# Kernel tuning notes

Hardware: AMD Instinct MI355X
Metric: run time of the kernel (lower is better)

The kernel has to match this reference:

```python
import jax, jax.numpy as jnp
import numpy as np

THETA = 10000.0

def _rope_cos_sin(seq_len, head_dim, dtype=jnp.float32):
    # matches precompute_freqs_cis: freqs over even indices of head_dim
    inv = 1.0 / (THETA ** (jnp.arange(0, head_dim, 2, dtype=jnp.float32) / head_dim))  # [hd/2]
    ang = jnp.arange(seq_len, dtype=jnp.float32)[:, None] * inv[None, :]               # [S, hd/2]
    return jnp.cos(ang).astype(dtype), jnp.sin(ang).astype(dtype)

def _apply_rope(x, cos, sin):
    # x: [b, h, s, d]; pairs are interleaved (d r) with r=2 -> complex (even=real, odd=imag)
    xe = x[..., 0::2]
    xo = x[..., 1::2]
    re = xe * cos - xo * sin
    im = xe * sin + xo * cos
    # interleave back: [..., d/2, 2] -> [..., d]
    return jnp.stack([re, im], axis=-1).reshape(x.shape)

def setup_inputs() -> dict:
    key = jax.random.key(0)
    ks = jax.random.split(key, 8)
    B, S, D = 2, 2048, 1024
    s = 0.02
    return {
        "query": jax.random.normal(ks[0], (B, S, D), jnp.float32),
        "key": jax.random.normal(ks[1], (B, S, D), jnp.float32),
        "value": jax.random.normal(ks[2], (B, S, D), jnp.float32),
        "q_w": jax.random.normal(ks[3], (D, D), jnp.float32) * s,
        "q_b": jnp.zeros((D,), jnp.float32),
        "k_w": jax.random.normal(ks[4], (D, D), jnp.float32) * s,
        "k_b": jnp.zeros((D,), jnp.float32),
        "v_w": jax.random.normal(ks[5], (D, D), jnp.float32) * s,
        "v_b": jnp.zeros((D,), jnp.float32),
        "o_w": jax.random.normal(ks[6], (D, D), jnp.float32) * s,
        "o_b": jnp.zeros((D,), jnp.float32),
    }

def reference(query, key, value, q_w, q_b, k_w, k_b, v_w, v_b, o_w, o_b):
    H = 16
    B, S, D = query.shape
    hd = D // H
    scaling = hd ** -0.5

    def split_heads(x):  # [b, s, (h d)] -> [b, h, s, d]
        return x.reshape(B, -1, H, hd).transpose(0, 2, 1, 3)

    q = split_heads(query @ q_w.T + q_b)
    k = split_heads(key @ k_w.T + k_b)
    v = split_heads(value @ v_w.T + v_b)

    cos, sin = _rope_cos_sin(S, hd)
    q = _apply_rope(q, cos, sin)
    k = _apply_rope(k, cos, sin)

    scores = jnp.einsum('bhqd,bhkd->bhqk', q, k) * scaling  # [B,H,S,S]
    attn = jax.nn.softmax(scores, axis=-1)
    out = jnp.einsum('bhqk,bhkd->bhqd', attn, v)            # [B,H,S,hd]
    out = out.transpose(0, 2, 1, 3).reshape(B, S, D)
    return out @ o_w.T + o_b
```

## Files before the change

### kernel.cpp

```cpp
#include <hip/hip_runtime.h>
#include <math.h>

#define B_  2
#define S_  2048
#define D_  1024
#define H_  16
#define HD_ 64
#define M_  (B_*S_)

typedef __attribute__((ext_vector_type(8))) short bf16x8;
typedef __attribute__((ext_vector_type(4))) short bf16x4;
typedef __attribute__((ext_vector_type(4))) float f32x4;
typedef unsigned short ushort_t;

#define MFMA32 __builtin_amdgcn_mfma_f32_16x16x32_bf16
#define MFMA16 __builtin_amdgcn_mfma_f32_16x16x16bf16_1k

__device__ inline unsigned short f2bf(float x) {
    unsigned u = __float_as_uint(x);
    unsigned r = (u + 0x7fff + ((u >> 16) & 1)) >> 16;
    return (unsigned short)r;
}
__device__ inline void gload16(const ushort_t* g, ushort_t* l) {
    __builtin_amdgcn_global_load_lds(
        (const __attribute__((address_space(1))) unsigned*)g,
        (__attribute__((address_space(3))) unsigned*)l, 16, 0, 0);
}

__global__ __launch_bounds__(256) void prep(
    const float* __restrict__ qa, const float* __restrict__ ka,
    const float* __restrict__ va,
    const float* __restrict__ qw, const float* __restrict__ kw,
    const float* __restrict__ vw, const float* __restrict__ ow,
    ushort_t* __restrict__ qab, ushort_t* __restrict__ kab,
    ushort_t* __restrict__ vab,
    ushort_t* __restrict__ qwb, ushort_t* __restrict__ kwb,
    ushort_t* __restrict__ vwb, ushort_t* __restrict__ owb,
    float* __restrict__ cost, float* __restrict__ sint)
{
    const int z = blockIdx.y;
    const int i = blockIdx.x * 256 + threadIdx.x;
    if (z == 7) {
        if (blockIdx.x >= (S_ * 32) / 256) return;
        int s = i >> 5, w = i & 31;
        double inv = pow(10000.0, -((double)(2 * w) / (double)HD_));
        double ang = (double)s * inv;
        cost[i] = (float)cos(ang);
        sint[i] = (float)sin(ang);
        return;
    }
    const float* in;
    ushort_t* dst;
    int n4;
    switch (z) {
        case 0: in = qa; dst = qab; n4 = (M_ * D_) / 4; break;
        case 1: in = ka; dst = kab; n4 = (M_ * D_) / 4; break;
        case 2: in = va; dst = vab; n4 = (M_ * D_) / 4; break;
        case 3: in = qw; dst = qwb; n4 = (D_ * D_) / 4; break;
        case 4: in = kw; dst = kwb; n4 = (D_ * D_) / 4; break;
        case 5: in = vw; dst = vwb; n4 = (D_ * D_) / 4; break;
        default: in = ow; dst = owb; n4 = (D_ * D_) / 4; break;
    }
    if (i >= n4) return;
    float4 v = ((const float4*)in)[i];
    unsigned short h0 = f2bf(v.x), h1 = f2bf(v.y), h2 = f2bf(v.z), h3 = f2bf(v.w);
    ((uint2*)dst)[i] = make_uint2((unsigned)h0 | ((unsigned)h1 << 16),
                                  (unsigned)h2 | ((unsigned)h3 << 16));
}

__global__ __launch_bounds__(256, 4) void fused_qkv(
    const ushort_t* __restrict__ A0, const ushort_t* __restrict__ A1,
    const ushort_t* __restrict__ A2,
    const ushort_t* __restrict__ W0, const ushort_t* __restrict__ W1,
    const ushort_t* __restrict__ W2,
    const float* __restrict__ b0, const float* __restrict__ b1,
    const float* __restrict__ b2,
    ushort_t* __restrict__ O0, ushort_t* __restrict__ O1,
    ushort_t* __restrict__ O2,
    const float* __restrict__ cost, const float* __restrict__ sint)
{
    __shared__ ushort_t Ab[4096];
    __shared__ ushort_t Wb[4096];

    const int tid  = threadIdx.x;
    const int wq   = tid >> 6;
    const int lane = tid & 63;
    const int l16  = lane & 15;
    const int quad = lane >> 4;
    const int bm   = blockIdx.y * 128;
    const int bn   = blockIdx.x * 128;
    const int z    = blockIdx.z;

    const ushort_t* A = z == 0 ? A0 : z == 1 ? A1 : A2;
    const ushort_t* W = z == 0 ? W0 : z == 1 ? W1 : W2;
    const float* bias = z == 0 ? b0 : z == 1 ? b1 : b2;

    const int m16 = tid & 15;
    const int akq = (tid >> 4) & 3;
    const int tw  = tid >> 6;

    const ushort_t* gA0 = A + (size_t)(bm + tw * 16 + m16) * D_ + akq * 8;
    const ushort_t* gA1 = gA0 + (size_t)64 * D_;
    const ushort_t* gW0 = W + (size_t)(bn + tw * 16 + m16) * D_ + akq * 8;
    const ushort_t* gW1 = gW0 + (size_t)64 * D_;

    ushort_t* lA0 = &Ab[tw * 512];
    ushort_t* lA1 = &Ab[(tw + 4) * 512];
    ushort_t* lW0 = &Wb[tw * 512];
    ushort_t* lW1 = &Wb[(tw + 4) * 512];

    const int wm = wq >> 1, wn = wq & 1;

    f32x4 acc[4][4];
#pragma unroll
    for (int mt = 0; mt < 4; ++mt)
#pragma unroll
        for (int nt = 0; nt < 4; ++nt)
            acc[mt][nt] = (f32x4){0.f, 0.f, 0.f, 0.f};

    for (int k0 = 0; k0 < D_; k0 += 32) {
        __syncthreads();
        gload16(gA0 + k0, lA0);
        gload16(gA1 + k0, lA1);
        gload16(gW0 + k0, lW0);
        gload16(gW1 + k0, lW1);
        __syncthreads();

        bf16x8 af[4], wf[4];
#pragma unroll
        for (int mt = 0; mt < 4; ++mt)
            af[mt] = *(const bf16x8*)&Ab[(wm * 4 + mt) * 512 + lane * 8];
#pragma unroll
        for (int nt = 0; nt < 4; ++nt)
            wf[nt] = *(const bf16x8*)&Wb[(wn * 4 + nt) * 512 + lane * 8];
#pragma unroll
        for (int mt = 0; mt < 4; ++mt)
#pragma unroll
            for (int nt = 0; nt < 4; ++nt)
                acc[mt][nt] = MFMA32(af[mt], wf[nt], acc[mt][nt], 0, 0, 0);
    }

    if (z == 0) {
        const float scale = 0.18033688011112042f;
#pragma unroll
        for (int mt = 0; mt < 4; ++mt) {
            int m = bm + wm * 64 + mt * 16 + quad * 4;
#pragma unroll
            for (int nt = 0; nt < 4; ++nt) {
                int n = bn + wn * 64 + nt * 16 + l16;
                float bb = bias[n];
                int h = n >> 6, d = n & 63, p = d >> 1;
#pragma unroll
                for (int r = 0; r < 4; ++r) {
                    int mm = m + r;
                    int s = mm & (S_ - 1), b = mm >> 11;
                    float x = acc[mt][nt][r] + bb;
                    float cs = cost[s * 32 + p], sn = sint[s * 32 + p];
                    float part = __shfl_xor(x, 1);
                    float y = (d & 1) ? (part * sn + x * cs)
                                      : (x * cs - part * sn);
                    O0[((size_t)(b * H_ + h) * S_ + s) * HD_ + d] = f2bf(y * scale);
                }
            }
        }
    } else if (z == 1) {
#pragma unroll
        for (int mt = 0; mt < 4; ++mt) {
            int m = bm + wm * 64 + mt * 16 + quad * 4;
#pragma unroll
            for (int nt = 0; nt < 4; ++nt) {
                int n = bn + wn * 64 + nt * 16 + l16;
                float bb = bias[n];
                int h = n >> 6, d = n & 63, p = d >> 1;
                int sub = ((d >> 5) & 1);
                int dq  = (d >> 3) & 3;
                int dj  = d & 7;
#pragma unroll
                for (int r = 0; r < 4; ++r) {
                    int mm = m + r;
                    int s = mm & (S_ - 1), b = mm >> 11;
                    float x = acc[mt][nt][r] + bb;
                    float cs = cost[s * 32 + p], sn = sint[s * 32 + p];
                    float part = __shfl_xor(x, 1);
                    float y = (d & 1) ? (part * sn + x * cs)
                                      : (x * cs - part * sn);
                    int kt  = s >> 5;
                    int st  = ((s >> 4) & 1) * 2 + sub;
                    size_t idx = ((size_t)(b * H_ + h) * 64 + kt) * 2048
                               + st * 512 + dq * 128 + (s & 15) * 8 + dj;
                    O1[idx] = f2bf(y);
                }
            }
        }
    } else {
#pragma unroll
        for (int mt = 0; mt < 4; ++mt) {
            int m = bm + wm * 64 + mt * 16 + quad * 4;
            int b = m >> 11, s0 = m & (S_ - 1);
            int vt = s0 >> 5;
            int kk = s0 & 31;
            int qd = (kk & 15) >> 2;
            int w0 = ((kk >> 4) & 1) * 4;
#pragma unroll
            for (int nt = 0; nt < 4; ++nt) {
                int n = bn + wn * 64 + nt * 16 + l16;
                float bb = bias[n];
                int h = n >> 6, d = n & 63;
                int mtv = d >> 4, dd = d & 15;
                unsigned short hh[4];
#pragma unroll
                for (int r = 0; r < 4; ++r)
                    hh[r] = f2bf(acc[mt][nt][r] + bb);
                size_t idx = ((size_t)(b * H_ + h) * 64 + vt) * 2048
                           + mtv * 512 + qd * 128 + dd * 8 + w0;
                *(uint2*)(O2 + idx) = make_uint2(
                    (unsigned)hh[0] | ((unsigned)hh[1] << 16),
                    (unsigned)hh[2] | ((unsigned)hh[3] << 16));
            }
        }
    }
}

__global__ __launch_bounds__(256, 4) void proj_o(
    const ushort_t* __restrict__ A, const ushort_t* __restrict__ W,
    const float* __restrict__ bias, float* __restrict__ outf)
{
    __shared__ ushort_t Ab[2048];
    __shared__ ushort_t Wb[4096];

    const int tid  = threadIdx.x;
    const int wq   = tid >> 6;
    const int lane = tid & 63;
    const int l16  = lane & 15;
    const int quad = lane >> 4;
    const int bm   = blockIdx.y * 64;
    const int bn   = blockIdx.x * 128;

    const int m16 = tid & 15;
    const int akq = (tid >> 4) & 3;
    const int tw  = tid >> 6;

    const ushort_t* gA  = A + (size_t)(bm + tw * 16 + m16) * D_ + akq * 8;
    const ushort_t* gW0 = W + (size_t)(bn + tw * 16 + m16) * D_ + akq * 8;
    const ushort_t* gW1 = gW0 + (size_t)64 * D_;

    ushort_t* lA  = &Ab[tw * 512];
    ushort_t* lW0 = &Wb[tw * 512];
    ushort_t* lW1 = &Wb[(tw + 4) * 512];

    const int wm = wq >> 1, wn = wq & 1;

    f32x4 acc[2][4];
#pragma unroll
    for (int mt = 0; mt < 2; ++mt)
#pragma unroll
        for (int nt = 0; nt < 4; ++nt)
            acc[mt][nt] = (f32x4){0.f, 0.f, 0.f, 0.f};

    for (int k0 = 0; k0 < D_; k0 += 32) {
        __syncthreads();
        gload16(gA + k0, lA);
        gload16(gW0 + k0, lW0);
        gload16(gW1 + k0, lW1);
        __syncthreads();

        bf16x8 af[2], wf[4];
#pragma unroll
        for (int mt = 0; mt < 2; ++mt)
            af[mt] = *(const bf16x8*)&Ab[(wm * 2 + mt) * 512 + lane * 8];
#pragma unroll
        for (int nt = 0; nt < 4; ++nt)
            wf[nt] = *(const bf16x8*)&Wb[(wn * 4 + nt) * 512 + lane * 8];
#pragma unroll
        for (int mt = 0; mt < 2; ++mt)
#pragma unroll
            for (int nt = 0; nt < 4; ++nt)
                acc[mt][nt] = MFMA32(af[mt], wf[nt], acc[mt][nt], 0, 0, 0);
    }

#pragma unroll
    for (int mt = 0; mt < 2; ++mt) {
        int m = bm + wm * 32 + mt * 16 + quad * 4;
#pragma unroll
        for (int nt = 0; nt < 4; ++nt) {
            int n = bn + wn * 64 + nt * 16 + l16;
            float bb = bias[n];
#pragma unroll
            for (int r = 0; r < 4; ++r)
                outf[(size_t)(m + r) * D_ + n] = acc[mt][nt][r] + bb;
        }
    }
}

__global__ __launch_bounds__(256, 2) void attn_mfma(
    const ushort_t* __restrict__ Q, const ushort_t* __restrict__ Kf,
    const ushort_t* __restrict__ Vf, ushort_t* __restrict__ AO)
{
    __shared__ ushort_t KS[4096];
    __shared__ ushort_t VS[4096];
    __shared__ float    MRG[128 * 65];
    __shared__ float    PSB[128];

    const int tid  = threadIdx.x;
    const int wq   = tid >> 6;
    const int lane = tid & 63;
    const int l16  = lane & 15;
    const int quad = lane >> 4;
    const int qg   = wq & 1;
    const int ks   = wq >> 1;
    const int bh   = blockIdx.y;
    const int q0   = blockIdx.x * 128 + qg * 64;

    bf16x8 qa[4][2];
#pragma unroll
    for (int nh = 0; nh < 4; ++nh)
#pragma unroll
        for (int c = 0; c < 2; ++c) {
            int row = q0 + nh * 16 + l16;
            qa[nh][c] = *(const bf16x8*)(Q + ((size_t)bh * S_ + row) * HD_
                                           + c * 32 + quad * 8);
        }

    f32x4 oacc[4][4];
    f32x4 osum[4];
#pragma unroll
    for (int nh = 0; nh < 4; ++nh) {
        osum[nh] = (f32x4){0.f, 0.f, 0.f, 0.f};
#pragma unroll
        for (int mt = 0; mt < 4; ++mt)
            oacc[nh][mt] = (f32x4){0.f, 0.f, 0.f, 0.f};
    }

    const bf16x4 ones = {(short)0x3F80, (short)0x3F80,
                         (short)0x3F80, (short)0x3F80};

    const ushort_t* Kp = Kf + (size_t)bh * 64 * 2048;
    const ushort_t* Vp = Vf + (size_t)bh * 64 * 2048;
    const ushort_t* Kc = KS + ks * 2048;
    const ushort_t* Vc = VS + ks * 2048;

    for (int i = 0; i < 32; ++i) {
        __syncthreads();
        gload16(Kp + tid * 8,        KS + tid * 8);
        gload16(Kp + 2048 + tid * 8, KS + 2048 + tid * 8);
        gload16(Vp + tid * 8,        VS + tid * 8);
        gload16(Vp + 2048 + tid * 8, VS + 2048 + tid * 8);
        Kp += 4096; Vp += 4096;
        __syncthreads();

        bf16x8 kf[2][2];
#pragma unroll
        for (int g = 0; g < 2; ++g)
#pragma unroll
            for (int c = 0; c < 2; ++c)
                kf[g][c] = *(const bf16x8*)&Kc[(g * 2 + c) * 512 + lane * 8];

        f32x4 s[4][2];
#pragma unroll
        for (int nh = 0; nh < 4; ++nh)
#pragma unroll
            for (int g = 0; g < 2; ++g)
                s[nh][g] = (f32x4){0.f, 0.f, 0.f, 0.f};
#pragma unroll
        for (int c = 0; c < 2; ++c)
#pragma unroll
            for (int nh = 0; nh < 4; ++nh)
#pragma unroll
                for (int g = 0; g < 2; ++g)
                    s[nh][g] = MFMA32(kf[g][c], qa[nh][c], s[nh][g], 0, 0, 0);

        bf16x4 pb[4][2];
#pragma unroll
        for (int nh = 0; nh < 4; ++nh)
#pragma unroll
            for (int g = 0; g < 2; ++g) {
                float p0 = __builtin_exp2f(s[nh][g][0]);
                float p1 = __builtin_exp2f(s[nh][g][1]);
                float p2 = __builtin_exp2f(s[nh][g][2]);
                float p3 = __builtin_exp2f(s[nh][g][3]);
                union { bf16x4 v; unsigned u[2]; } t;
                t.u[0] = __builtin_amdgcn_perm(__float_as_uint(p1),
                                               __float_as_uint(p0), 0x07060302);
                t.u[1] = __builtin_amdgcn_perm(__float_as_uint(p3),
                                               __float_as_uint(p2), 0x07060302);
                pb[nh][g] = t.v;
            }

#pragma unroll
        for (int mt = 0; mt < 4; ++mt) {
            bf16x8 vv = *(const bf16x8*)&Vc[mt * 512 + lane * 8];
            bf16x4 v0 = __builtin_shufflevector(vv, vv, 0, 1, 2, 3);
            bf16x4 v1 = __builtin_shufflevector(vv, vv, 4, 5, 6, 7);
#pragma unroll
            for (int nh = 0; nh < 4; ++nh) {
                oacc[nh][mt] = MFMA16(v0, pb[nh][0], oacc[nh][mt], 0, 0, 0);
                oacc[nh][mt] = MFMA16(v1, pb[nh][1], oacc[nh][mt], 0, 0, 0);
            }
        }
#pragma unroll
        for (int nh = 0; nh < 4; ++nh) {
            osum[nh] = MFMA16(ones, pb[nh][0], osum[nh], 0, 0, 0);
            osum[nh] = MFMA16(ones, pb[nh][1], osum[nh], 0, 0, 0);
        }
    }

    if (ks == 1) {
#pragma unroll
        for (int nh = 0; nh < 4; ++nh) {
#pragma unroll
            for (int mt = 0; mt < 4; ++mt)
#pragma unroll
                for (int r = 0; r < 4; ++r)
                    MRG[(qg * 64 + nh * 16 + l16) * 65 + mt * 16 + quad * 4 + r]
                        = oacc[nh][mt][r];
            if (quad == 0)
                PSB[qg * 64 + nh * 16 + l16] = osum[nh][0];
        }
    }
    __syncthreads();
    if (ks == 0) {
        const int b = bh >> 4, h = bh & 15;
#pragma unroll
        for (int nh = 0; nh < 4; ++nh) {
            float pst = osum[nh][0] + PSB[qg * 64 + nh * 16 + l16];
            float inv = 1.0f / pst;
            int q = q0 + nh * 16 + l16;
#pragma unroll
            for (int mt = 0; mt < 4; ++mt) {
                unsigned short hh[4];
#pragma unroll
                for (int r = 0; r < 4; ++r) {
                    float x = oacc[nh][mt][r]
                        + MRG[(qg * 64 + nh * 16 + l16) * 65 + mt * 16 + quad * 4 + r];
                    hh[r] = f2bf(x * inv);
                }
                size_t base = ((size_t)b * S_ + q) * D_ + h * HD_
                            + mt * 16 + quad * 4;
                *(uint2*)(AO + base) = make_uint2(
                    (unsigned)hh[0] | ((unsigned)hh[1] << 16),
                    (unsigned)hh[2] | ((unsigned)hh[3] << 16));
            }
        }
    }
}

extern "C" void kernel_launch(void* const* d_in, const int* in_sizes, int n_in,
                              void* d_out, int out_size, void* d_ws, size_t ws_size,
                              hipStream_t stream) {
    const float* query = (const float*)d_in[0];
    const float* key   = (const float*)d_in[1];
    const float* value = (const float*)d_in[2];
    const float* q_w   = (const float*)d_in[3];
    const float* q_b   = (const float*)d_in[4];
    const float* k_w   = (const float*)d_in[5];
    const float* k_b   = (const float*)d_in[6];
    const float* v_w   = (const float*)d_in[7];
    const float* v_b   = (const float*)d_in[8];
    const float* o_w   = (const float*)d_in[9];
    const float* o_b   = (const float*)d_in[10];
    float* out = (float*)d_out;

    const size_t NT = (size_t)M_ * D_;
    const size_t WT = (size_t)D_ * D_;
    ushort_t* p = (ushort_t*)d_ws;
    ushort_t* qa_b = p; p += NT;
    ushort_t* ka_b = p; p += NT;
    ushort_t* va_b = p; p += NT;
    ushort_t* wqb  = p; p += WT;
    ushort_t* wkb  = p; p += WT;
    ushort_t* wvb  = p; p += WT;
    ushort_t* wob  = p; p += WT;
    ushort_t* Qb   = p; p += NT;
    ushort_t* Kfr  = p; p += NT;
    ushort_t* Vfr  = p; p += NT;
    ushort_t* AO   = p; p += NT;
    float* cost = (float*)p;
    float* sint = cost + (size_t)S_ * 32;

    dim3 gp((unsigned)(NT / 4 / 256), 8);
    prep<<<gp, 256, 0, stream>>>(query, key, value, q_w, k_w, v_w, o_w,
                                 qa_b, ka_b, va_b, wqb, wkb, wvb, wob,
                                 cost, sint);

    dim3 gq(D_ / 128, M_ / 128, 3);
    fused_qkv<<<gq, 256, 0, stream>>>(
        qa_b, ka_b, va_b, wqb, wkb, wvb,
        q_b, k_b, v_b, Qb, Kfr, Vfr, cost, sint);

    dim3 agrid(S_ / 128, B_ * H_);
    attn_mfma<<<agrid, 256, 0, stream>>>(Qb, Kfr, Vfr, AO);

    dim3 go(D_ / 128, M_ / 64);
    proj_o<<<go, 256, 0, stream>>>(AO, wob, o_b, out);
}
```

Before: 257.7 us.

## Double-buffer LDS tiles in GEMMs and attention; merge PV MFMAs into 16x16x32

All three kernels (QKV projection, output projection, attention) now use double-buffered LDS tiles. The next K-slice is prefetched with global_load_lds while the current slice is being computed, which drops one barrier per iteration. The attention kernel also replaces pairs of 16x16x16 bf16 MFMAs for P·V and the row-sum with single 16x16x32 MFMAs, packing P into bf16x8 fragments. It overlays the merge buffer onto the K/V buffers to fit the larger LDS footprint. Launch-bound occupancy hints are lowered to match the larger shared memory, which risks fewer waves per CU.

```diff
diff --git a/kernel.cpp b/kernel.cpp
--- a/kernel.cpp
+++ b/kernel.cpp
@@ -9,12 +9,10 @@
 #define M_  (B_*S_)
 
 typedef __attribute__((ext_vector_type(8))) short bf16x8;
-typedef __attribute__((ext_vector_type(4))) short bf16x4;
 typedef __attribute__((ext_vector_type(4))) float f32x4;
 typedef unsigned short ushort_t;
 
 #define MFMA32 __builtin_amdgcn_mfma_f32_16x16x32_bf16
-#define MFMA16 __builtin_amdgcn_mfma_f32_16x16x16bf16_1k
 
 __device__ inline unsigned short f2bf(float x) {
     unsigned u = __float_as_uint(x);
@@ -68,7 +66,7 @@
                                   (unsigned)h2 | ((unsigned)h3 << 16));
 }
 
-__global__ __launch_bounds__(256, 4) void fused_qkv(
+__global__ __launch_bounds__(256, 3) void fused_qkv(
     const ushort_t* __restrict__ A0, const ushort_t* __restrict__ A1,
     const ushort_t* __restrict__ A2,
     const ushort_t* __restrict__ W0, const ushort_t* __restrict__ W1,
@@ -79,8 +77,8 @@
     ushort_t* __restrict__ O2,
     const float* __restrict__ cost, const float* __restrict__ sint)
 {
-    __shared__ ushort_t Ab[4096];
-    __shared__ ushort_t Wb[4096];
+    __shared__ ushort_t Ab[8192];
+    __shared__ ushort_t Wb[8192];
 
     const int tid  = threadIdx.x;
     const int wq   = tid >> 6;
@@ -104,11 +102,6 @@
     const ushort_t* gW0 = W + (size_t)(bn + tw * 16 + m16) * D_ + akq * 8;
     const ushort_t* gW1 = gW0 + (size_t)64 * D_;
 
-    ushort_t* lA0 = &Ab[tw * 512];
-    ushort_t* lA1 = &Ab[(tw + 4) * 512];
-    ushort_t* lW0 = &Wb[tw * 512];
-    ushort_t* lW1 = &Wb[(tw + 4) * 512];
-
     const int wm = wq >> 1, wn = wq & 1;
 
     f32x4 acc[4][4];
@@ -118,26 +111,37 @@
         for (int nt = 0; nt < 4; ++nt)
             acc[mt][nt] = (f32x4){0.f, 0.f, 0.f, 0.f};
 
+    gload16(gA0, &Ab[tw * 512]);
+    gload16(gA1, &Ab[(tw + 4) * 512]);
+    gload16(gW0, &Wb[tw * 512]);
+    gload16(gW1, &Wb[(tw + 4) * 512]);
+    __syncthreads();
+
     for (int k0 = 0; k0 < D_; k0 += 32) {
-        __syncthreads();
-        gload16(gA0 + k0, lA0);
-        gload16(gA1 + k0, lA1);
-        gload16(gW0 + k0, lW0);
-        gload16(gW1 + k0, lW1);
-        __syncthreads();
+        const int cur = (k0 >> 5) & 1;
+        if (k0 + 32 < D_) {
+            const int nxt = cur ^ 1;
+            gload16(gA0 + k0 + 32, &Ab[nxt * 4096 + tw * 512]);
+            gload16(gA1 + k0 + 32, &Ab[nxt * 4096 + (tw + 4) * 512]);
+            gload16(gW0 + k0 + 32, &Wb[nxt * 4096 + tw * 512]);
+            gload16(gW1 + k0 + 32, &Wb[nxt * 4096 + (tw + 4) * 512]);
+        }
+        const ushort_t* Abc = &Ab[cur * 4096];
+        const ushort_t* Wbc = &Wb[cur * 4096];
 
         bf16x8 af[4], wf[4];
 #pragma unroll
         for (int mt = 0; mt < 4; ++mt)
-            af[mt] = *(const bf16x8*)&Ab[(wm * 4 + mt) * 512 + lane * 8];
+            af[mt] = *(const bf16x8*)&Abc[(wm * 4 + mt) * 512 + lane * 8];
 #pragma unroll
         for (int nt = 0; nt < 4; ++nt)
-            wf[nt] = *(const bf16x8*)&Wb[(wn * 4 + nt) * 512 + lane * 8];
+            wf[nt] = *(const bf16x8*)&Wbc[(wn * 4 + nt) * 512 + lane * 8];
 #pragma unroll
         for (int mt = 0; mt < 4; ++mt)
 #pragma unroll
             for (int nt = 0; nt < 4; ++nt)
                 acc[mt][nt] = MFMA32(af[mt], wf[nt], acc[mt][nt], 0, 0, 0);
+        __syncthreads();
     }
 
     if (z == 0) {
@@ -221,12 +225,12 @@
     }
 }
 
-__global__ __launch_bounds__(256, 4) void proj_o(
+__global__ __launch_bounds__(256, 2) void proj_o(
     const ushort_t* __restrict__ A, const ushort_t* __restrict__ W,
     const float* __restrict__ bias, float* __restrict__ outf)
 {
-    __shared__ ushort_t Ab[2048];
-    __shared__ ushort_t Wb[4096];
+    __shared__ ushort_t Ab[4096];
+    __shared__ ushort_t Wb[8192];
 
     const int tid  = threadIdx.x;
     const int wq   = tid >> 6;
@@ -244,10 +248,6 @@
     const ushort_t* gW0 = W + (size_t)(bn + tw * 16 + m16) * D_ + akq * 8;
     const ushort_t* gW1 = gW0 + (size_t)64 * D_;
 
-    ushort_t* lA  = &Ab[tw * 512];
-    ushort_t* lW0 = &Wb[tw * 512];
-    ushort_t* lW1 = &Wb[(tw + 4) * 512];
-
     const int wm = wq >> 1, wn = wq & 1;
 
     f32x4 acc[2][4];
@@ -257,25 +257,35 @@
         for (int nt = 0; nt < 4; ++nt)
             acc[mt][nt] = (f32x4){0.f, 0.f, 0.f, 0.f};
 
+    gload16(gA,  &Ab[tw * 512]);
+    gload16(gW0, &Wb[tw * 512]);
+    gload16(gW1, &Wb[(tw + 4) * 512]);
+    __syncthreads();
+
     for (int k0 = 0; k0 < D_; k0 += 32) {
-        __syncthreads();
-        gload16(gA + k0, lA);
-        gload16(gW0 + k0, lW0);
-        gload16(gW1 + k0, lW1);
-        __syncthreads();
+        const int cur = (k0 >> 5) & 1;
+        if (k0 + 32 < D_) {
+            const int nxt = cur ^ 1;
+            gload16(gA  + k0 + 32, &Ab[nxt * 2048 + tw * 512]);
+            gload16(gW0 + k0 + 32, &Wb[nxt * 4096 + tw * 512]);
+            gload16(gW1 + k0 + 32, &Wb[nxt * 4096 + (tw + 4) * 512]);
+        }
+        const ushort_t* Abc = &Ab[cur * 2048];
+        const ushort_t* Wbc = &Wb[cur * 4096];
 
         bf16x8 af[2], wf[4];
 #pragma unroll
         for (int mt = 0; mt < 2; ++mt)
-            af[mt] = *(const bf16x8*)&Ab[(wm * 2 + mt) * 512 + lane * 8];
+            af[mt] = *(const bf16x8*)&Abc[(wm * 2 + mt) * 512 + lane * 8];
 #pragma unroll
         for (int nt = 0; nt < 4; ++nt)
-            wf[nt] = *(const bf16x8*)&Wb[(wn * 4 + nt) * 512 + lane * 8];
+            wf[nt] = *(const bf16x8*)&Wbc[(wn * 4 + nt) * 512 + lane * 8];
 #pragma unroll
         for (int mt = 0; mt < 2; ++mt)
 #pragma unroll
             for (int nt = 0; nt < 4; ++nt)
                 acc[mt][nt] = MFMA32(af[mt], wf[nt], acc[mt][nt], 0, 0, 0);
+        __syncthreads();
     }
 
 #pragma unroll
@@ -296,10 +306,11 @@
     const ushort_t* __restrict__ Q, const ushort_t* __restrict__ Kf,
     const ushort_t* __restrict__ Vf, ushort_t* __restrict__ AO)
 {
-    __shared__ ushort_t KS[4096];
-    __shared__ ushort_t VS[4096];
-    __shared__ float    MRG[128 * 65];
-    __shared__ float    PSB[128];
+    __shared__ __align__(16) unsigned char SM[33280 + 512];
+    ushort_t* KS  = (ushort_t*)SM;
+    ushort_t* VS  = (ushort_t*)(SM + 16384);
+    float*    MRG = (float*)SM;
+    float*    PSB = (float*)(SM + 33280);
 
     const int tid  = threadIdx.x;
     const int wq   = tid >> 6;
@@ -331,22 +342,32 @@
             oacc[nh][mt] = (f32x4){0.f, 0.f, 0.f, 0.f};
     }
 
-    const bf16x4 ones = {(short)0x3F80, (short)0x3F80,
-                         (short)0x3F80, (short)0x3F80};
+    const bf16x8 ones8 = {(short)0x3F80, (short)0x3F80, (short)0x3F80,
+                          (short)0x3F80, (short)0x3F80, (short)0x3F80,
+                          (short)0x3F80, (short)0x3F80};
 
     const ushort_t* Kp = Kf + (size_t)bh * 64 * 2048;
     const ushort_t* Vp = Vf + (size_t)bh * 64 * 2048;
-    const ushort_t* Kc = KS + ks * 2048;
-    const ushort_t* Vc = VS + ks * 2048;
+
+    gload16(Kp + tid * 8,        KS + tid * 8);
+    gload16(Kp + 2048 + tid * 8, KS + 2048 + tid * 8);
+    gload16(Vp + tid * 8,        VS + tid * 8);
+    gload16(Vp + 2048 + tid * 8, VS + 2048 + tid * 8);
+    Kp += 4096; Vp += 4096;
+    __syncthreads();
 
     for (int i = 0; i < 32; ++i) {
-        __syncthreads();
-        gload16(Kp + tid * 8,        KS + tid * 8);
-        gload16(Kp + 2048 + tid * 8, KS + 2048 + tid * 8);
-        gload16(Vp + tid * 8,        VS + tid * 8);
-        gload16(Vp + 2048 + tid * 8, VS + 2048 + tid * 8);
-        Kp += 4096; Vp += 4096;
-        __syncthreads();
+        const int cur = i & 1;
+        if (i < 31) {
+            const int nxt = cur ^ 1;
+            gload16(Kp + tid * 8,        KS + nxt * 4096 + tid * 8);
+            gload16(Kp + 2048 + tid * 8, KS + nxt * 4096 + 2048 + tid * 8);
+            gload16(Vp + tid * 8,        VS + nxt * 4096 + tid * 8);
+            gload16(Vp + 2048 + tid * 8, VS + nxt * 4096 + 2048 + tid * 8);
+            Kp += 4096; Vp += 4096;
+        }
+        const ushort_t* Kc = KS + cur * 4096 + ks * 2048;
+        const ushort_t* Vc = VS + cur * 4096 + ks * 2048;
 
         bf16x8 kf[2][2];
 #pragma unroll
@@ -369,39 +390,41 @@
                 for (int g = 0; g < 2; ++g)
                     s[nh][g] = MFMA32(kf[g][c], qa[nh][c], s[nh][g], 0, 0, 0);
 
-        bf16x4 pb[4][2];
-#pragma unroll
-        for (int nh = 0; nh < 4; ++nh)
-#pragma unroll
-            for (int g = 0; g < 2; ++g) {
-                float p0 = __builtin_exp2f(s[nh][g][0]);
-                float p1 = __builtin_exp2f(s[nh][g][1]);
-                float p2 = __builtin_exp2f(s[nh][g][2]);
-                float p3 = __builtin_exp2f(s[nh][g][3]);
-                union { bf16x4 v; unsigned u[2]; } t;
-                t.u[0] = __builtin_amdgcn_perm(__float_as_uint(p1),
-                                               __float_as_uint(p0), 0x07060302);
-                t.u[1] = __builtin_amdgcn_perm(__float_as_uint(p3),
-                                               __float_as_uint(p2), 0x07060302);
-                pb[nh][g] = t.v;
-            }
+        bf16x8 pb8[4];
+#pragma unroll
+        for (int nh = 0; nh < 4; ++nh) {
+            float p00 = __builtin_exp2f(s[nh][0][0]);
+            float p01 = __builtin_exp2f(s[nh][0][1]);
+            float p02 = __builtin_exp2f(s[nh][0][2]);
+            float p03 = __builtin_exp2f(s[nh][0][3]);
+            float p10 = __builtin_exp2f(s[nh][1][0]);
+            float p11 = __builtin_exp2f(s[nh][1][1]);
+            float p12 = __builtin_exp2f(s[nh][1][2]);
+            float p13 = __builtin_exp2f(s[nh][1][3]);
+            union { bf16x8 v; unsigned u[4]; } t;
+            t.u[0] = __builtin_amdgcn_perm(__float_as_uint(p01),
+                                           __float_as_uint(p00), 0x07060302);
+            t.u[1] = __builtin_amdgcn_perm(__float_as_uint(p03),
+                                           __float_as_uint(p02), 0x07060302);
+            t.u[2] = __builtin_amdgcn_perm(__float_as_uint(p11),
+                                           __float_as_uint(p10), 0x07060302);
+            t.u[3] = __builtin_amdgcn_perm(__float_as_uint(p13),
+                                           __float_as_uint(p12), 0x07060302);
+            pb8[nh] = t.v;
+        }
 
 #pragma unroll
         for (int mt = 0; mt < 4; ++mt) {
             bf16x8 vv = *(const bf16x8*)&Vc[mt * 512 + lane * 8];
-            bf16x4 v0 = __builtin_shufflevector(vv, vv, 0, 1, 2, 3);
-            bf16x4 v1 = __builtin_shufflevector(vv, vv, 4, 5, 6, 7);
-#pragma unroll
-            for (int nh = 0; nh < 4; ++nh) {
-                oacc[nh][mt] = MFMA16(v0, pb[nh][0], oacc[nh][mt], 0, 0, 0);
-                oacc[nh][mt] = MFMA16(v1, pb[nh][1], oacc[nh][mt], 0, 0, 0);
-            }
-        }
-#pragma unroll
-        for (int nh = 0; nh < 4; ++nh) {
-            osum[nh] = MFMA16(ones, pb[nh][0], osum[nh], 0, 0, 0);
-            osum[nh] = MFMA16(ones, pb[nh][1], osum[nh], 0, 0, 0);
-        }
+#pragma unroll
+            for (int nh = 0; nh < 4; ++nh)
+                oacc[nh][mt] = MFMA32(vv, pb8[nh], oacc[nh][mt], 0, 0, 0);
+        }
+#pragma unroll
+        for (int nh = 0; nh < 4; ++nh)
+            osum[nh] = MFMA32(ones8, pb8[nh], osum[nh], 0, 0, 0);
+
+        __syncthreads();
     }
 
     if (ks == 1) {
```

Result: no change. 254.2 us (-1.4%).
